# Kernel tuning notes

Hardware: AMD Instinct MI355X
Metric: run time of the kernel (lower is better)

## Reference

```python
import jax, jax.numpy as jnp
import numpy as np

LAMBDA_COE = 0.5
EPS = 1e-12  # F.normalize default eps


def setup_inputs() -> dict:
    key = jax.random.key(0)
    k1, k2, k3 = jax.random.split(key, 3)
    B, C = 8192, 2
    D, N = 1024, 8192
    outputs = jax.random.normal(k1, (B, C), dtype=jnp.float32)
    labels = jax.random.randint(k2, (B,), 0, C, dtype=jnp.int64)
    H = jax.random.normal(k3, (D, N), dtype=jnp.float32)
    return {"outputs": outputs, "labels": labels, "H": H}


def reference(outputs, labels, H):
    # --- pairwise cosine-similarity regularizer over columns of H ---
    Ht = H.T                                   # [N, D]
    N = Ht.shape[0]
    norms = jnp.maximum(jnp.linalg.norm(Ht, axis=1, keepdims=True), EPS)
    Hn = Ht / norms                            # row-normalized [N, D]
    G = Hn @ Hn.T                              # [N, N] cosine sims
    # sum over strict upper triangle = (sum(G) - trace(G)) / 2
    pair_sum = (jnp.sum(G) - jnp.trace(G)) * 0.5
    reg_term = pair_sum * LAMBDA_COE / (N * (N - 1) / 2)

    # --- cross-entropy (mean reduction), matching nn.CrossEntropyLoss ---
    logp = jax.nn.log_softmax(outputs, axis=-1)          # [B, C]
    nll = -jnp.take_along_axis(logp, labels[:, None], axis=1)[:, 0]
    ce = jnp.mean(nll)

    return ce + reg_term
```

## Files before the change

### kernel.cpp

```cpp
#include <hip/hip_runtime.h>
#include <math.h>


#define N_COLS  8192
#define D_ROWS  1024
#define B_ROWS  8192
#define ROWS_PER_BLOCK 16
#define EPS_NORM 1e-12f

__device__ inline float block_reduce_sum_256(float v) {
    #pragma unroll
    for (int off = 32; off > 0; off >>= 1) v += __shfl_down(v, off, 64);
    __shared__ float sm[4];
    int lane = threadIdx.x & 63;
    int wid  = threadIdx.x >> 6;
    if (lane == 0) sm[wid] = v;
    __syncthreads();
    if (threadIdx.x < 4) {
        v = sm[threadIdx.x];
        v += __shfl_down(v, 2, 64);
        v += __shfl_down(v, 1, 64);
    }
    return v;
}

__global__ __launch_bounds__(256)
void colsumsq_kernel(const float* __restrict__ H, float* __restrict__ norms2) {
    const int col4 = blockIdx.x * blockDim.x + threadIdx.x;
    const int row0 = blockIdx.y * ROWS_PER_BLOCK;
    const float4* __restrict__ H4 = (const float4*)H;
    float ax = 0.f, ay = 0.f, az = 0.f, aw = 0.f;
    #pragma unroll
    for (int r = 0; r < ROWS_PER_BLOCK; ++r) {
        float4 v = H4[(size_t)(row0 + r) * (N_COLS / 4) + col4];
        ax = fmaf(v.x, v.x, ax);
        ay = fmaf(v.y, v.y, ay);
        az = fmaf(v.z, v.z, az);
        aw = fmaf(v.w, v.w, aw);
    }
    const int col = col4 * 4;
    atomicAdd(&norms2[col + 0], ax);
    atomicAdd(&norms2[col + 1], ay);
    atomicAdd(&norms2[col + 2], az);
    atomicAdd(&norms2[col + 3], aw);
}

__global__ __launch_bounds__(256)
void gemv_s2_kernel(const float* __restrict__ H, const float* __restrict__ norms2,
                    float* __restrict__ s2_acc) {
    const int d = blockIdx.x;
    const float4* __restrict__ Hrow = (const float4*)(H + (size_t)d * N_COLS);
    const float4* __restrict__ n24  = (const float4*)norms2;
    float acc = 0.f;
    #pragma unroll 4
    for (int i = threadIdx.x; i < N_COLS / 4; i += 256) {
        float4 v  = Hrow[i];
        float4 n2 = n24[i];
        float wx = 1.f / fmaxf(sqrtf(n2.x), EPS_NORM);
        float wy = 1.f / fmaxf(sqrtf(n2.y), EPS_NORM);
        float wz = 1.f / fmaxf(sqrtf(n2.z), EPS_NORM);
        float ww = 1.f / fmaxf(sqrtf(n2.w), EPS_NORM);
        acc = fmaf(v.x, wx, acc);
        acc = fmaf(v.y, wy, acc);
        acc = fmaf(v.z, wz, acc);
        acc = fmaf(v.w, ww, acc);
    }
    float s = block_reduce_sum_256(acc);
    if (threadIdx.x == 0) atomicAdd(s2_acc, s * s);
}

__global__ __launch_bounds__(256)
void ce_kernel(const float* __restrict__ logits, const int* __restrict__ labels,
               float* __restrict__ ce_acc) {
    const int b = blockIdx.x * blockDim.x + threadIdx.x;
    float2 x = ((const float2*)logits)[b];
    float m = fmaxf(x.x, x.y);
    float lse = m + logf(expf(x.x - m) + expf(x.y - m));
    int lab = labels[b];
    float xl = (lab == 0) ? x.x : x.y;
    float nll = lse - xl;
    float s = block_reduce_sum_256(nll);
    if (threadIdx.x == 0) atomicAdd(ce_acc, s);
}

__global__ void finalize_kernel(const float* __restrict__ s2_acc,
                                const float* __restrict__ ce_acc,
                                float* __restrict__ out) {
    double s2 = (double)s2_acc[0];
    double reg = (s2 - (double)N_COLS) * 0.5 / ((double)N_COLS * (double)(N_COLS - 1));
    double ce = (double)ce_acc[0] / (double)B_ROWS;
    out[0] = (float)(ce + reg);
}

extern "C" void kernel_launch(void* const* d_in, const int* in_sizes, int n_in,
                              void* d_out, int out_size, void* d_ws, size_t ws_size,
                              hipStream_t stream) {
    const float* outputs = (const float*)d_in[0];
    const int*   labels  = (const int*)d_in[1];
    const float* H       = (const float*)d_in[2];
    float* out = (float*)d_out;

    float* norms2 = (float*)d_ws;
    float* s2_acc = norms2 + N_COLS;
    float* ce_acc = s2_acc + 1;

    hipMemsetAsync(d_ws, 0, (N_COLS + 2) * sizeof(float), stream);

    colsumsq_kernel<<<dim3(N_COLS / 1024, D_ROWS / ROWS_PER_BLOCK), 256, 0, stream>>>(H, norms2);
    gemv_s2_kernel<<<D_ROWS, 256, 0, stream>>>(H, norms2, s2_acc);
    ce_kernel<<<B_ROWS / 256, 256, 0, stream>>>(outputs, labels, ce_acc);
    finalize_kernel<<<1, 1, 0, stream>>>(s2_acc, ce_acc, out);
}
```

Baseline: 111.7 us.

## Fuse CE into column-norm kernel and finalize into GEMV via last-block counter

Merges the cross-entropy computation into the column-sum-of-squares kernel as extra blocks, and folds the finalize step into the GEMV kernel using an atomic done-counter so the last block writes the output. The number of kernel launches drops from four to two. It also doubles the rows per column-norm block, which halves the atomics on norms2, and replaces sqrt+divide with rsqrtf and fast exp/log intrinsics. In exchange it adds a threadfence and a counter atomic in every GEMV block, and the fast math intrinsics slightly lower precision.

```diff
diff --git a/kernel.cpp b/kernel.cpp
--- a/kernel.cpp
+++ b/kernel.cpp
@@ -5,8 +5,10 @@
 #define N_COLS  8192
 #define D_ROWS  1024
 #define B_ROWS  8192
-#define ROWS_PER_BLOCK 16
-#define EPS_NORM 1e-12f
+#define CSS_BLOCKS   256
+#define CSS_ROWS_PER  32
+#define CE_BLOCKS    32
+#define GEMV_BLOCKS  1024
 
 __device__ inline float block_reduce_sum_256(float v) {
     #pragma unroll
@@ -25,71 +27,78 @@
 }
 
 __global__ __launch_bounds__(256)
-void colsumsq_kernel(const float* __restrict__ H, float* __restrict__ norms2) {
-    const int col4 = blockIdx.x * blockDim.x + threadIdx.x;
-    const int row0 = blockIdx.y * ROWS_PER_BLOCK;
-    const float4* __restrict__ H4 = (const float4*)H;
-    float ax = 0.f, ay = 0.f, az = 0.f, aw = 0.f;
-    #pragma unroll
-    for (int r = 0; r < ROWS_PER_BLOCK; ++r) {
-        float4 v = H4[(size_t)(row0 + r) * (N_COLS / 4) + col4];
-        ax = fmaf(v.x, v.x, ax);
-        ay = fmaf(v.y, v.y, ay);
-        az = fmaf(v.z, v.z, az);
-        aw = fmaf(v.w, v.w, aw);
+void colsumsq_ce_kernel(const float* __restrict__ H,
+                        const float* __restrict__ logits,
+                        const int* __restrict__ labels,
+                        float* __restrict__ norms2,
+                        float* __restrict__ ce_acc) {
+    if (blockIdx.x < CSS_BLOCKS) {
+        const int cg = blockIdx.x & 7;
+        const int rg = blockIdx.x >> 3;
+        const int col4 = cg * 256 + threadIdx.x;
+        const int row0 = rg * CSS_ROWS_PER;
+        const float4* __restrict__ H4 = (const float4*)H;
+        float ax = 0.f, ay = 0.f, az = 0.f, aw = 0.f;
+        #pragma unroll
+        for (int r = 0; r < CSS_ROWS_PER; ++r) {
+            float4 v = H4[(size_t)(row0 + r) * (N_COLS / 4) + col4];
+            ax = fmaf(v.x, v.x, ax);
+            ay = fmaf(v.y, v.y, ay);
+            az = fmaf(v.z, v.z, az);
+            aw = fmaf(v.w, v.w, aw);
+        }
+        const int col = col4 * 4;
+        atomicAdd(&norms2[col + 0], ax);
+        atomicAdd(&norms2[col + 1], ay);
+        atomicAdd(&norms2[col + 2], az);
+        atomicAdd(&norms2[col + 3], aw);
+    } else {
+        const int b = (blockIdx.x - CSS_BLOCKS) * 256 + threadIdx.x;
+        float2 x = ((const float2*)logits)[b];
+        float m = fmaxf(x.x, x.y);
+        float lse = m + __logf(__expf(x.x - m) + __expf(x.y - m));
+        float xl = (labels[b] == 0) ? x.x : x.y;
+        float s = block_reduce_sum_256(lse - xl);
+        if (threadIdx.x == 0) atomicAdd(ce_acc, s);
     }
-    const int col = col4 * 4;
-    atomicAdd(&norms2[col + 0], ax);
-    atomicAdd(&norms2[col + 1], ay);
-    atomicAdd(&norms2[col + 2], az);
-    atomicAdd(&norms2[col + 3], aw);
 }
 
 __global__ __launch_bounds__(256)
-void gemv_s2_kernel(const float* __restrict__ H, const float* __restrict__ norms2,
-                    float* __restrict__ s2_acc) {
+void gemv_s2_finalize_kernel(const float* __restrict__ H,
+                             const float* __restrict__ norms2,
+                             float* __restrict__ s2_acc,
+                             const float* __restrict__ ce_acc,
+                             unsigned int* __restrict__ done_cnt,
+                             float* __restrict__ out) {
     const int d = blockIdx.x;
     const float4* __restrict__ Hrow = (const float4*)(H + (size_t)d * N_COLS);
     const float4* __restrict__ n24  = (const float4*)norms2;
     float acc = 0.f;
-    #pragma unroll 4
+    #pragma unroll
     for (int i = threadIdx.x; i < N_COLS / 4; i += 256) {
         float4 v  = Hrow[i];
         float4 n2 = n24[i];
-        float wx = 1.f / fmaxf(sqrtf(n2.x), EPS_NORM);
-        float wy = 1.f / fmaxf(sqrtf(n2.y), EPS_NORM);
-        float wz = 1.f / fmaxf(sqrtf(n2.z), EPS_NORM);
-        float ww = 1.f / fmaxf(sqrtf(n2.w), EPS_NORM);
-        acc = fmaf(v.x, wx, acc);
-        acc = fmaf(v.y, wy, acc);
-        acc = fmaf(v.z, wz, acc);
-        acc = fmaf(v.w, ww, acc);
+        acc = fmaf(v.x, rsqrtf(fmaxf(n2.x, 1e-24f)), acc);
+        acc = fmaf(v.y, rsqrtf(fmaxf(n2.y, 1e-24f)), acc);
+        acc = fmaf(v.z, rsqrtf(fmaxf(n2.z, 1e-24f)), acc);
+        acc = fmaf(v.w, rsqrtf(fmaxf(n2.w, 1e-24f)), acc);
     }
     float s = block_reduce_sum_256(acc);
-    if (threadIdx.x == 0) atomicAdd(s2_acc, s * s);
-}
-
-__global__ __launch_bounds__(256)
-void ce_kernel(const float* __restrict__ logits, const int* __restrict__ labels,
-               float* __restrict__ ce_acc) {
-    const int b = blockIdx.x * blockDim.x + threadIdx.x;
-    float2 x = ((const float2*)logits)[b];
-    float m = fmaxf(x.x, x.y);
-    float lse = m + logf(expf(x.x - m) + expf(x.y - m));
-    int lab = labels[b];
-    float xl = (lab == 0) ? x.x : x.y;
-    float nll = lse - xl;
-    float s = block_reduce_sum_256(nll);
-    if (threadIdx.x == 0) atomicAdd(ce_acc, s);
-}
-
-__global__ void finalize_kernel(const float* __restrict__ s2_acc,
-                                const float* __restrict__ ce_acc,
-                                float* __restrict__ out) {
-    double s2 = (double)s2_acc[0];
-    double reg = (s2 - (double)N_COLS) * 0.5 / ((double)N_COLS * (double)(N_COLS - 1));
-    double ce = (double)ce_acc[0] / (double)B_ROWS;
-    out[0] = (float)(ce + reg);
+    __shared__ bool last;
+    if (threadIdx.x == 0) {
+        atomicAdd(s2_acc, s * s);
+        __threadfence();
+        unsigned int old = atomicAdd(done_cnt, 1u);
+        last = (old == GEMV_BLOCKS - 1);
+    }
+    __syncthreads();
+    if (last && threadIdx.x == 0) {
+        float s2 = atomicAdd(s2_acc, 0.f);
+        float ce = atomicAdd((float*)ce_acc, 0.f);
+        double reg = ((double)s2 - (double)N_COLS) * 0.5
+                     / ((double)N_COLS * (double)(N_COLS - 1));
+        out[0] = (float)((double)ce / (double)B_ROWS + reg);
+    }
 }
 
 extern "C" void kernel_launch(void* const* d_in, const int* in_sizes, int n_in,
@@ -103,11 +112,12 @@
     float* norms2 = (float*)d_ws;
     float* s2_acc = norms2 + N_COLS;
     float* ce_acc = s2_acc + 1;
+    unsigned int* done_cnt = (unsigned int*)(ce_acc + 1);
 
-    hipMemsetAsync(d_ws, 0, (N_COLS + 2) * sizeof(float), stream);
+    hipMemsetAsync(d_ws, 0, (N_COLS + 3) * sizeof(float), stream);
 
-    colsumsq_kernel<<<dim3(N_COLS / 1024, D_ROWS / ROWS_PER_BLOCK), 256, 0, stream>>>(H, norms2);
-    gemv_s2_kernel<<<D_ROWS, 256, 0, stream>>>(H, norms2, s2_acc);
-    ce_kernel<<<B_ROWS / 256, 256, 0, stream>>>(outputs, labels, ce_acc);
-    finalize_kernel<<<1, 1, 0, stream>>>(s2_acc, ce_acc, out);
+    colsumsq_ce_kernel<<<CSS_BLOCKS + CE_BLOCKS, 256, 0, stream>>>(
+        H, outputs, labels, norms2, ce_acc);
+    gemv_s2_finalize_kernel<<<GEMV_BLOCKS, 256, 0, stream>>>(
+        H, norms2, s2_acc, ce_acc, done_cnt, out);
 }
```

Measured after the change: 117.2 us. +5.0%, slower.
